# Optimization experiments

Measured on AMD Instinct MI355X. Metric: run time of the kernel, lower is better.

The kernel has to match this reference:

```python
import jax, jax.numpy as jnp
import numpy as np

HID = 1024
H = 8
HD = HID // H  # 128; KV length must equal HD for the bias-add broadcast
B = 8
LQ = 4096
LK = HD


def setup_inputs() -> dict:
    key = jax.random.key(0)
    ks = jax.random.split(key, 16)
    s = 0.02
    inp = {
        "query": jax.random.normal(ks[0], (B, LQ, HID), jnp.float32),
        "key": jax.random.normal(ks[1], (B, LK, HID), jnp.float32),
        "value": jax.random.normal(ks[2], (B, LK, HID), jnp.float32),
        "atten": jax.random.normal(ks[3], (B, LQ, HID), jnp.float32),
        "mask": jax.random.randint(ks[4], (B, 1, 1, LK), 0, 2, jnp.int32),
        "Wq": jax.random.normal(ks[5], (HID, HID), jnp.float32) * s,
        "bq": jnp.zeros((HID,), jnp.float32),
        "Wk": jax.random.normal(ks[6], (HID, HID), jnp.float32) * s,
        "bk": jnp.zeros((HID,), jnp.float32),
        "Wv": jax.random.normal(ks[7], (HID, HID), jnp.float32) * s,
        "bv": jnp.zeros((HID,), jnp.float32),
        "Watt": jax.random.normal(ks[8], (HID, HID), jnp.float32) * s,
        "batt": jnp.zeros((HID,), jnp.float32),
        "Wfc": jax.random.normal(ks[9], (HID, HID), jnp.float32) * s,
        "bfc": jnp.zeros((HID,), jnp.float32),
    }
    return inp


def _heads(x):
    # [B, L, HID] -> [B, H, L, HD]
    b, l, _ = x.shape
    return x.reshape(b, l, H, HD).transpose(0, 2, 1, 3)


def reference(query, key, value, atten, mask, Wq, bq, Wk, bk, Wv, bv, Watt, batt, Wfc, bfc):
    scale = jnp.sqrt(jnp.asarray(HD, jnp.float32))
    atten_out = _heads(atten @ Watt.T + batt)          # [B,H,LQ,HD]
    Q = _heads(query @ Wq.T + bq)                      # [B,H,LQ,HD]
    K = _heads(key @ Wk.T + bk)                        # [B,H,LK,HD]
    V = _heads(value @ Wv.T + bv)                      # [B,H,LK,HD]
    energy = jnp.einsum('bhqd,bhkd->bhqk', Q, K) / scale + atten_out  # LK == HD
    energy = jnp.where(mask == 0, jnp.float32(-1e10), energy)
    attention = jax.nn.softmax(energy, axis=-1)
    x = jnp.einsum('bhqk,bhkd->bhqd', attention, V)
    x = x.transpose(0, 2, 1, 3).reshape(query.shape[0], -1, HID)
    return x @ Wfc.T + bfc
```

## Files before the change

kernel.cpp:

```cpp
#include <hip/hip_runtime.h>
#include <hip/hip_bf16.h>
#include <stdint.h>

typedef __bf16 bf16_t;
typedef __bf16 bf16x8 __attribute__((ext_vector_type(8)));
typedef __bf16 bf16x4 __attribute__((ext_vector_type(4)));
typedef float f32x4 __attribute__((ext_vector_type(4)));

#define HIDN 1024
#define NHEAD 8
#define HDIM 128
#define NBATCH 8
#define LQLEN 4096
#define LKLEN 128

__device__ __forceinline__ void gload_lds16(const void* g, void* l) {
  __builtin_amdgcn_global_load_lds(
      (const __attribute__((address_space(1))) unsigned int*)g,
      (__attribute__((address_space(3))) unsigned int*)l, 16, 0, 0);
}

__global__ __launch_bounds__(256) void convk(const float* __restrict__ in,
                                             bf16_t* __restrict__ out, int n4) {
  int i = blockIdx.x * blockDim.x + threadIdx.x;
  const int stride = gridDim.x * blockDim.x;
  for (; i < n4; i += stride) {
    const float4 v = ((const float4*)in)[i];
    bf16x4 o;
    o[0] = (bf16_t)v.x; o[1] = (bf16_t)v.y; o[2] = (bf16_t)v.z; o[3] = (bf16_t)v.w;
    ((bf16x4*)out)[i] = o;
  }
}

template <int MODE>
__global__ __launch_bounds__(512, 2) void gemm8p(const bf16_t* __restrict__ A,
                                                 const bf16_t* __restrict__ Bw,
                                                 const float* __restrict__ bias,
                                                 void* __restrict__ Cout) {
  constexpr int NT = 32;
  constexpr int SLOT = 32768;
  __shared__ uint4 smem_raw[8192];
  char* smem = (char*)smem_raw;

  const int tid = threadIdx.x;
  const int wid = tid >> 6, lane = tid & 63;
  const int lr = lane & 15, lh = lane >> 4;
  const int wr = wid >> 2, wc = wid & 3;

  const int bid = blockIdx.x;
  const int m_blk = (bid & 7) * 16 + (bid >> 5);
  const int n_blk = (bid >> 3) & 3;
  const int m0 = m_blk * 256, n0 = n_blk * 256;

  const int c0 = tid, c1 = tid + 512;
  const int sc0 = (((c0 & 3) ^ ((c0 >> 3) & 3)) << 4);
  const int sc1 = (((c1 & 3) ^ ((c1 >> 3) & 3)) << 4);
  const char* srcA0 = (const char*)A + (size_t)(m0 + (c0 >> 2)) * 2048 + sc0;
  const char* srcA1 = (const char*)A + (size_t)(m0 + (c1 >> 2)) * 2048 + sc1;
  const char* srcB0 = (const char*)Bw + (size_t)(n0 + (c0 >> 2)) * 2048 + sc0;
  const char* srcB1 = (const char*)Bw + (size_t)(n0 + (c1 >> 2)) * 2048 + sc1;
  const int d0 = c0 * 16, d1 = c1 * 16;

  f32x4 acc[8][4] = {};

#pragma unroll
  for (int tt = 0; tt < 3; ++tt) {
    char* dst = smem + tt * SLOT;
    gload_lds16(srcA0 + tt * 64, dst + d0);
    gload_lds16(srcA1 + tt * 64, dst + d1);
    gload_lds16(srcB0 + tt * 64, dst + 16384 + d0);
    gload_lds16(srcB1 + tt * 64, dst + 16384 + d1);
  }
  asm volatile("s_waitcnt vmcnt(8)" ::: "memory");
  __builtin_amdgcn_s_barrier();

  const int swz = ((lr >> 1) & 3) << 4;
  const int aoff = (wr * 128 + lr) * 64 + ((lh << 4) ^ swz);
  const int boff = 16384 + (wc * 64 + lr) * 64 + ((lh << 4) ^ swz);

  for (int t = 0; t < NT; ++t) {
    const char* sA = smem + (t & 3) * SLOT + aoff;
    const char* sB = smem + (t & 3) * SLOT + boff;
    char* dst = smem + ((t + 3) & 3) * SLOT;
    const int kb = (t + 3) * 64;
    const bool pf = (t <= NT - 4);

    bf16x8 bfr[4], af0[4];
#pragma unroll
    for (int n = 0; n < 4; ++n) bfr[n] = *(const bf16x8*)(sB + n * 1024);
#pragma unroll
    for (int m = 0; m < 4; ++m) af0[m] = *(const bf16x8*)(sA + m * 1024);
    if (pf) {
      gload_lds16(srcA0 + kb, dst + d0);
      gload_lds16(srcA1 + kb, dst + d1);
    }
    __builtin_amdgcn_s_barrier();
    asm volatile("s_waitcnt lgkmcnt(0)" ::: "memory");
    __builtin_amdgcn_sched_barrier(0);
    __builtin_amdgcn_s_setprio(1);
#pragma unroll
    for (int m = 0; m < 4; ++m)
#pragma unroll
      for (int n = 0; n < 4; ++n)
        acc[m][n] = __builtin_amdgcn_mfma_f32_16x16x32_bf16(af0[m], bfr[n], acc[m][n], 0, 0, 0);
    __builtin_amdgcn_s_setprio(0);
    __builtin_amdgcn_s_barrier();

    bf16x8 af1[4];
#pragma unroll
    for (int m = 0; m < 4; ++m) af1[m] = *(const bf16x8*)(sA + (m + 4) * 1024);
    if (pf) {
      gload_lds16(srcB0 + kb, dst + 16384 + d0);
      gload_lds16(srcB1 + kb, dst + 16384 + d1);
    }
    __builtin_amdgcn_s_barrier();
    asm volatile("s_waitcnt lgkmcnt(0)" ::: "memory");
    __builtin_amdgcn_sched_barrier(0);
    __builtin_amdgcn_s_setprio(1);
#pragma unroll
    for (int m = 0; m < 4; ++m)
#pragma unroll
      for (int n = 0; n < 4; ++n)
        acc[m + 4][n] = __builtin_amdgcn_mfma_f32_16x16x32_bf16(af1[m], bfr[n], acc[m + 4][n], 0, 0, 0);
    __builtin_amdgcn_s_setprio(0);

    if (t < NT - 1) {
      __builtin_amdgcn_sched_barrier(0);
      if (t <= NT - 4)
        asm volatile("s_waitcnt vmcnt(8)" ::: "memory");
      else if (t == NT - 3)
        asm volatile("s_waitcnt vmcnt(4)" ::: "memory");
      else
        asm volatile("s_waitcnt vmcnt(0)" ::: "memory");
      __builtin_amdgcn_sched_barrier(0);
      __builtin_amdgcn_s_barrier();
    }
  }

  if constexpr (MODE == 2) {
    float* C = (float*)Cout;
#pragma unroll
    for (int f = 0; f < 8; ++f) {
      const int gm = m0 + wr * 128 + f * 16 + lh * 4;
#pragma unroll
      for (int j = 0; j < 4; ++j) {
        const int gn = n0 + wc * 64 + j * 16 + lr;
        const float bb = bias[gn];
#pragma unroll
        for (int r = 0; r < 4; ++r)
          C[(size_t)(gm + r) * HIDN + gn] = acc[f][j][r] + bb;
      }
    }
  } else {
    bf16_t* C = (bf16_t*)Cout;
#pragma unroll
    for (int f = 0; f < 8; ++f) {
      const int gm = m0 + wr * 128 + f * 16 + lh * 4;
#pragma unroll
      for (int j = 0; j < 4; ++j) {
        const int gn = n0 + wc * 64 + j * 16 + lr;
        const float bb = bias[gn];
        const int h = gn >> 7, d = gn & 127;
#pragma unroll
        for (int r = 0; r < 4; ++r) {
          const int b = (gm + r) >> 12, l = (gm + r) & 4095;
          C[(((size_t)(b * NHEAD + h) * LQLEN + l) << 7) + d] = (bf16_t)(acc[f][j][r] + bb);
        }
      }
    }
  }
}

template <int MODE, int LROW>
__global__ __launch_bounds__(256) void gemm_bt(const bf16_t* __restrict__ A,
                                               const bf16_t* __restrict__ Bw,
                                               const float* __restrict__ bias,
                                               void* __restrict__ Cout) {
  constexpr int BK = 32;
  __shared__ uint4 AsRaw[128 * BK * 2 / 16];
  __shared__ uint4 BsRaw[128 * BK * 2 / 16];
  bf16_t* As = (bf16_t*)AsRaw;
  bf16_t* Bs = (bf16_t*)BsRaw;

  const int tid = threadIdx.x;
  const int wid = tid >> 6;
  const int lane = tid & 63;
  const int lr = lane & 15, lh = lane >> 4;
  const int m0 = blockIdx.x * 128, n0 = blockIdx.y * 128;
  const int wm = (wid >> 1) * 64, wn = (wid & 1) * 64;

  f32x4 acc[4][4] = {};

  const int srow = lane >> 2;
  const int scol = (lane & 3) * 16;

  for (int k0 = 0; k0 < HIDN; k0 += BK) {
#pragma unroll
    for (int i = 0; i < 2; ++i) {
      const int c = wid + i * 4;
      const int row = c * 16 + srow;
      gload_lds16((const char*)A + ((size_t)(m0 + row) * HIDN + k0) * 2 + scol,
                  (char*)As + c * 1024);
      gload_lds16((const char*)Bw + ((size_t)(n0 + row) * HIDN + k0) * 2 + scol,
                  (char*)Bs + c * 1024);
    }
    __syncthreads();

    bf16x8 af[4], bfr[4];
#pragma unroll
    for (int i = 0; i < 4; ++i) {
      af[i]  = *(const bf16x8*)(As + (wm + i * 16 + lr) * BK + lh * 8);
      bfr[i] = *(const bf16x8*)(Bs + (wn + i * 16 + lr) * BK + lh * 8);
    }
#pragma unroll
    for (int i = 0; i < 4; ++i)
#pragma unroll
      for (int j = 0; j < 4; ++j)
        acc[i][j] = __builtin_amdgcn_mfma_f32_16x16x32_bf16(af[i], bfr[j], acc[i][j], 0, 0, 0);
    __syncthreads();
  }

#pragma unroll
  for (int i = 0; i < 4; ++i) {
#pragma unroll
    for (int r = 0; r < 4; ++r) {
      const int gm = m0 + wm + i * 16 + lh * 4 + r;
#pragma unroll
      for (int j = 0; j < 4; ++j) {
        const int gn = n0 + wn + j * 16 + lr;
        const float v = acc[i][j][r] + bias[gn];
        const int b = gm / LROW, l = gm - b * LROW;
        const int h = gn >> 7, d = gn & 127;
        size_t idx;
        if constexpr (MODE == 0)
          idx = (((size_t)(b * NHEAD + h) * LROW + l) << 7) + d;
        else
          idx = (((size_t)(b * NHEAD + h) * 128 + d) << 7) + l;
        ((bf16_t*)Cout)[idx] = (bf16_t)v;
      }
    }
  }
}

__global__ __launch_bounds__(256) void attn_kernel(
    const bf16_t* __restrict__ Qh, const bf16_t* __restrict__ Ah,
    const bf16_t* __restrict__ Kh, const bf16_t* __restrict__ Vt,
    const int* __restrict__ mask, bf16_t* __restrict__ X) {
  __shared__ uint4 KsRaw[2048];
  __shared__ uint4 VsRaw[2048];
  __shared__ float Ms[128];
  char* Ks = (char*)KsRaw;
  char* Vs = (char*)VsRaw;

  const int tid = threadIdx.x, wid = tid >> 6, lane = tid & 63;
  const int lr = lane & 15, lh = lane >> 4;
  const int bh = blockIdx.y, b = bh >> 3, h = bh & 7;
  const int q0 = blockIdx.x * 64;

  {
    const char* Kg = (const char*)(Kh + (size_t)bh * 16384);
    const char* Vg = (const char*)(Vt + (size_t)bh * 16384);
#pragma unroll
    for (int it = 0; it < 8; ++it) {
      const int e = it * 256 + tid;
      const int row = e >> 4;
      const int cb = (e & 15) << 4;
      const int dst = row * 256 + (cb ^ ((row & 7) << 4));
      *(uint4*)(Ks + dst) = *(const uint4*)(Kg + row * 256 + cb);
      *(uint4*)(Vs + dst) = *(const uint4*)(Vg + row * 256 + cb);
    }
  }
  if (tid < 128) Ms[tid] = (mask[b * 128 + tid] == 0) ? 0.f : 1.f;

  bf16x8 qf[4];
  {
    const bf16_t* Qb = Qh + ((size_t)bh * LQLEN + q0 + wid * 16 + lr) * 128;
#pragma unroll
    for (int s = 0; s < 4; ++s) qf[s] = *(const bf16x8*)(Qb + s * 32 + lh * 8);
  }
  __syncthreads();

  f32x4 acc[8] = {};
#pragma unroll
  for (int nt = 0; nt < 8; ++nt) {
#pragma unroll
    for (int s = 0; s < 4; ++s) {
      const int row = nt * 16 + lr;
      const int cb = (s * 64 + lh * 16) ^ ((row & 7) << 4);
      const bf16x8 kf = *(const bf16x8*)(Ks + row * 256 + cb);
      acc[nt] = __builtin_amdgcn_mfma_f32_16x16x32_bf16(qf[s], kf, acc[nt], 0, 0, 0);
    }
  }

  float ex[8][4];
  float rsum[4];
  const float sc = 0.08838834764831845f;
  const bf16_t* Ab = Ah + ((size_t)bh * LQLEN + q0 + wid * 16) * 128;
#pragma unroll
  for (int r = 0; r < 4; ++r) {
    const int row = lh * 4 + r;
    float mx = -3.0e38f;
#pragma unroll
    for (int nt = 0; nt < 8; ++nt) {
      const int col = nt * 16 + lr;
      float e = acc[nt][r] * sc + (float)Ab[row * 128 + col];
      e = (Ms[col] != 0.f) ? e : -1.0e10f;
      ex[nt][r] = e;
      mx = fmaxf(mx, e);
    }
    mx = fmaxf(mx, __shfl_xor(mx, 1));
    mx = fmaxf(mx, __shfl_xor(mx, 2));
    mx = fmaxf(mx, __shfl_xor(mx, 4));
    mx = fmaxf(mx, __shfl_xor(mx, 8));
    float s_ = 0.f;
#pragma unroll
    for (int nt = 0; nt < 8; ++nt) {
      const float p = expf(ex[nt][r] - mx);
      ex[nt][r] = p;
      s_ += p;
    }
    s_ += __shfl_xor(s_, 1);
    s_ += __shfl_xor(s_, 2);
    s_ += __shfl_xor(s_, 4);
    s_ += __shfl_xor(s_, 8);
    rsum[r] = s_;
  }

  __syncthreads();
  char* Pb = Ks + wid * 4096;
#pragma unroll
  for (int r = 0; r < 4; ++r) {
    const int row = lh * 4 + r;
#pragma unroll
    for (int nt = 0; nt < 8; ++nt) {
      const int col = nt * 16 + lr;
      const int off = (row * 256 + col * 2) ^ ((row & 7) << 4);
      *(bf16_t*)(Pb + off) = (bf16_t)ex[nt][r];
    }
  }
  __syncthreads();

  bf16x8 pf[4];
#pragma unroll
  for (int s = 0; s < 4; ++s)
    pf[s] = *(const bf16x8*)(Pb + lr * 256 + ((s * 64 + lh * 16) ^ ((lr & 7) << 4)));
  f32x4 acc2[8] = {};
#pragma unroll
  for (int nt = 0; nt < 8; ++nt) {
#pragma unroll
    for (int s = 0; s < 4; ++s) {
      const int row = nt * 16 + lr;
      const int cb = (s * 64 + lh * 16) ^ ((row & 7) << 4);
      const bf16x8 vf = *(const bf16x8*)(Vs + row * 256 + cb);
      acc2[nt] = __builtin_amdgcn_mfma_f32_16x16x32_bf16(pf[s], vf, acc2[nt], 0, 0, 0);
    }
  }

  float rs[4];
#pragma unroll
  for (int r = 0; r < 4; ++r) rs[r] = 1.f / rsum[r];
  bf16_t* Xb = X + ((size_t)b * LQLEN + q0 + wid * 16) * HIDN + h * 128;
#pragma unroll
  for (int nt = 0; nt < 8; ++nt)
#pragma unroll
    for (int r = 0; r < 4; ++r)
      Xb[(size_t)(lh * 4 + r) * HIDN + nt * 16 + lr] = (bf16_t)(acc2[nt][r] * rs[r]);
}

extern "C" void kernel_launch(void* const* d_in, const int* in_sizes, int n_in,
                              void* d_out, int out_size, void* d_ws, size_t ws_size,
                              hipStream_t stream) {
  const float* query = (const float*)d_in[0];
  const float* key   = (const float*)d_in[1];
  const float* value = (const float*)d_in[2];
  const float* atten = (const float*)d_in[3];
  const int*   mask  = (const int*)d_in[4];
  const float* Wq  = (const float*)d_in[5];  const float* bq   = (const float*)d_in[6];
  const float* Wk  = (const float*)d_in[7];  const float* bk   = (const float*)d_in[8];
  const float* Wv  = (const float*)d_in[9];  const float* bv   = (const float*)d_in[10];
  const float* Wat = (const float*)d_in[11]; const float* batt = (const float*)d_in[12];
  const float* Wfc = (const float*)d_in[13]; const float* bfc  = (const float*)d_in[14];

  char* ws = (char*)d_ws;
  bf16_t* qbf = (bf16_t*)(ws + 0x0000000);
  bf16_t* abf = (bf16_t*)(ws + 0x4000000);
  bf16_t* Qh  = (bf16_t*)(ws + 0x8000000);
  bf16_t* Ah  = (bf16_t*)(ws + 0xC000000);
  char* sm = ws + 0x10000000;
  bf16_t* kbf = (bf16_t*)(sm + 0x000000);
  bf16_t* vbf = (bf16_t*)(sm + 0x200000);
  bf16_t* wqb = (bf16_t*)(sm + 0x400000);
  bf16_t* wkb = (bf16_t*)(sm + 0x600000);
  bf16_t* wvb = (bf16_t*)(sm + 0x800000);
  bf16_t* wab = (bf16_t*)(sm + 0xA00000);
  bf16_t* wfb = (bf16_t*)(sm + 0xC00000);
  bf16_t* Kh  = (bf16_t*)(sm + 0xE00000);
  bf16_t* Vt  = (bf16_t*)(sm + 0x1000000);
  bf16_t* X   = qbf;

  auto conv = [&](const float* src, bf16_t* dst, int n) {
    const int n4 = n >> 2;
    int g = (n4 + 255) >> 8; if (g > 2048) g = 2048;
    convk<<<dim3(g), dim3(256), 0, stream>>>(src, dst, n4);
  };
  conv(query, qbf, NBATCH * LQLEN * HIDN);
  conv(atten, abf, NBATCH * LQLEN * HIDN);
  conv(key,   kbf, NBATCH * LKLEN * HIDN);
  conv(value, vbf, NBATCH * LKLEN * HIDN);
  conv(Wq,  wqb, HIDN * HIDN);
  conv(Wk,  wkb, HIDN * HIDN);
  conv(Wv,  wvb, HIDN * HIDN);
  conv(Wat, wab, HIDN * HIDN);
  conv(Wfc, wfb, HIDN * HIDN);

  gemm_bt<0, 128><<<dim3(8, 8), dim3(256), 0, stream>>>(kbf, wkb, bk, (void*)Kh);
  gemm_bt<1, 128><<<dim3(8, 8), dim3(256), 0, stream>>>(vbf, wvb, bv, (void*)Vt);

  gemm8p<0><<<dim3(512), dim3(512), 0, stream>>>(qbf, wqb, bq, (void*)Qh);
  gemm8p<0><<<dim3(512), dim3(512), 0, stream>>>(abf, wab, batt, (void*)Ah);

  attn_kernel<<<dim3(LQLEN / 64, NBATCH * NHEAD), dim3(256), 0, stream>>>(
      Qh, Ah, Kh, Vt, mask, X);

  gemm8p<2><<<dim3(512), dim3(512), 0, stream>>>(X, wfb, bfc, d_out);
}
```

Baseline: 464.9 us.

## Merge GEMM k-step into single MFMA phase and stage bf16 epilogue through LDS

The main loop now loads all eight A fragments and issues every prefetch at once, running a single 32-MFMA block per k-step instead of two halves separated by barriers. This cuts the per-iteration barrier and waitcnt overhead but raises register pressure. The bf16 head-layout epilogue now writes the tile to per-wave LDS first, then stores 16-byte vectors to global memory instead of scattered 2-byte stores. The LDS staging reuses the pipeline buffer after a final barrier.

```diff
diff --git a/kernel.cpp b/kernel.cpp
--- a/kernel.cpp
+++ b/kernel.cpp
@@ -73,6 +73,7 @@
   }
   asm volatile("s_waitcnt vmcnt(8)" ::: "memory");
   __builtin_amdgcn_s_barrier();
+  __builtin_amdgcn_sched_barrier(0);
 
   const int swz = ((lr >> 1) & 3) << 4;
   const int aoff = (wr * 128 + lr) * 64 + ((lh << 4) ^ swz);
@@ -85,43 +86,23 @@
     const int kb = (t + 3) * 64;
     const bool pf = (t <= NT - 4);
 
-    bf16x8 bfr[4], af0[4];
+    bf16x8 bfr[4], af[8];
 #pragma unroll
     for (int n = 0; n < 4; ++n) bfr[n] = *(const bf16x8*)(sB + n * 1024);
 #pragma unroll
-    for (int m = 0; m < 4; ++m) af0[m] = *(const bf16x8*)(sA + m * 1024);
+    for (int m = 0; m < 8; ++m) af[m] = *(const bf16x8*)(sA + m * 1024);
     if (pf) {
       gload_lds16(srcA0 + kb, dst + d0);
       gload_lds16(srcA1 + kb, dst + d1);
-    }
-    __builtin_amdgcn_s_barrier();
-    asm volatile("s_waitcnt lgkmcnt(0)" ::: "memory");
-    __builtin_amdgcn_sched_barrier(0);
-    __builtin_amdgcn_s_setprio(1);
-#pragma unroll
-    for (int m = 0; m < 4; ++m)
-#pragma unroll
-      for (int n = 0; n < 4; ++n)
-        acc[m][n] = __builtin_amdgcn_mfma_f32_16x16x32_bf16(af0[m], bfr[n], acc[m][n], 0, 0, 0);
-    __builtin_amdgcn_s_setprio(0);
-    __builtin_amdgcn_s_barrier();
-
-    bf16x8 af1[4];
-#pragma unroll
-    for (int m = 0; m < 4; ++m) af1[m] = *(const bf16x8*)(sA + (m + 4) * 1024);
-    if (pf) {
       gload_lds16(srcB0 + kb, dst + 16384 + d0);
       gload_lds16(srcB1 + kb, dst + 16384 + d1);
     }
-    __builtin_amdgcn_s_barrier();
-    asm volatile("s_waitcnt lgkmcnt(0)" ::: "memory");
-    __builtin_amdgcn_sched_barrier(0);
     __builtin_amdgcn_s_setprio(1);
 #pragma unroll
-    for (int m = 0; m < 4; ++m)
+    for (int m = 0; m < 8; ++m)
 #pragma unroll
       for (int n = 0; n < 4; ++n)
-        acc[m + 4][n] = __builtin_amdgcn_mfma_f32_16x16x32_bf16(af1[m], bfr[n], acc[m + 4][n], 0, 0, 0);
+        acc[m][n] = __builtin_amdgcn_mfma_f32_16x16x32_bf16(af[m], bfr[n], acc[m][n], 0, 0, 0);
     __builtin_amdgcn_s_setprio(0);
 
     if (t < NT - 1) {
@@ -132,8 +113,8 @@
         asm volatile("s_waitcnt vmcnt(4)" ::: "memory");
       else
         asm volatile("s_waitcnt vmcnt(0)" ::: "memory");
+      __builtin_amdgcn_s_barrier();
       __builtin_amdgcn_sched_barrier(0);
-      __builtin_amdgcn_s_barrier();
     }
   }
 
@@ -152,21 +133,35 @@
       }
     }
   } else {
-    bf16_t* C = (bf16_t*)Cout;
+    __builtin_amdgcn_s_barrier();
+    __builtin_amdgcn_sched_barrier(0);
+    char* wlds = smem + wid * 16384;
 #pragma unroll
     for (int f = 0; f < 8; ++f) {
-      const int gm = m0 + wr * 128 + f * 16 + lh * 4;
 #pragma unroll
       for (int j = 0; j < 4; ++j) {
         const int gn = n0 + wc * 64 + j * 16 + lr;
         const float bb = bias[gn];
-        const int h = gn >> 7, d = gn & 127;
-#pragma unroll
-        for (int r = 0; r < 4; ++r) {
-          const int b = (gm + r) >> 12, l = (gm + r) & 4095;
-          C[(((size_t)(b * NHEAD + h) * LQLEN + l) << 7) + d] = (bf16_t)(acc[f][j][r] + bb);
-        }
+#pragma unroll
+        for (int r = 0; r < 4; ++r)
+          *(bf16_t*)(wlds + (f * 16 + lh * 4 + r) * 128 + (j * 16 + lr) * 2) =
+              (bf16_t)(acc[f][j][r] + bb);
       }
+    }
+    asm volatile("s_waitcnt lgkmcnt(0)" ::: "memory");
+    __builtin_amdgcn_sched_barrier(0);
+    bf16_t* C = (bf16_t*)Cout;
+    const int gnb = n0 + wc * 64;
+    const int h = gnb >> 7, dd = gnb & 127;
+#pragma unroll
+    for (int p = 0; p < 16; ++p) {
+      const int rl = p * 8 + (lane >> 3);
+      const int cb = (lane & 7) * 16;
+      const uint4 v = *(const uint4*)(wlds + rl * 128 + cb);
+      const int gm = m0 + wr * 128 + rl;
+      const int b = gm >> 12, l = gm & 4095;
+      char* dstp = (char*)(C + (((size_t)(b * NHEAD + h) * LQLEN + l) << 7) + dd) + cb;
+      *(uint4*)dstp = v;
     }
   }
 }
```

After: 466.8 us. Within noise of the previous version (+0.4%).
